# Kernel tuning notes

Measured on AMD Instinct MI355X. Metric: run time of the kernel, lower is better.

## Reference

```python
import jax, jax.numpy as jnp
import numpy as np

EPS = 1e-5

def _layernorm(x, gamma, beta):
    # normalize over last (channel) axis, per point
    mu = jnp.mean(x, axis=-1, keepdims=True)
    var = jnp.mean(jnp.square(x - mu), axis=-1, keepdims=True)
    return (x - mu) * jax.lax.rsqrt(var + EPS) * gamma + beta

def setup_inputs() -> dict:
    key = jax.random.key(0)
    ks = jax.random.split(key, 12)
    B, N, C, F = 32, 4096, 3, 1024
    points = jax.random.normal(ks[0], (B, N, C), dtype=jnp.float32)
    mask = jax.random.randint(ks[1], (B, 1, N), 0, 2, dtype=jnp.int32)
    s = 0.05
    return {
        "points": points,
        "mask": mask,
        "w1": jax.random.normal(ks[2], (128, C), dtype=jnp.float32) * s,      # conv1 (no bias)
        "g1": jnp.ones((128,), jnp.float32),                                   # norm1 gamma
        "be1": jnp.zeros((128,), jnp.float32),                                 # norm1 beta
        "w2": jax.random.normal(ks[3], (256, 128), dtype=jnp.float32) * s,     # conv2
        "b2": jax.random.normal(ks[4], (256,), dtype=jnp.float32) * s,
        "w3": jax.random.normal(ks[5], (512, 512), dtype=jnp.float32) * s,     # conv3 (no bias)
        "g2": jnp.ones((512,), jnp.float32),                                   # norm2 gamma
        "be2": jnp.zeros((512,), jnp.float32),                                 # norm2 beta
        "w4": jax.random.normal(ks[6], (F, 512), dtype=jnp.float32) * s,       # conv4
        "b4": jax.random.normal(ks[7], (F,), dtype=jnp.float32) * s,
    }

def reference(points, mask, w1, g1, be1, w2, b2, w3, g2, be2, w4, b4):
    # points: [B, N, C]; mask: [B, 1, N]
    vis = (mask[:, 0, :] != 0).astype(points.dtype)[..., None]  # [B, N, 1]
    # conv1 (1x1, no bias) as point-wise matmul
    h0 = jnp.einsum('bnc,kc->bnk', points, w1)                  # [B, N, 128]
    # masked LayerNorm: LN is per-point over channels, so compute densely and zero invisible points
    h1 = _layernorm(h0, g1, be1) * vis
    h2 = jax.nn.relu(h1)
    h3 = jnp.einsum('bnk,ok->bno', h2, w2) + b2                 # [B, N, 256]
    gmax = jnp.max(h3, axis=1, keepdims=True)                   # [B, 1, 256]
    dist = jnp.concatenate([jnp.broadcast_to(gmax, h3.shape), h3], axis=-1)  # [B, N, 512]
    h4 = jnp.einsum('bno,po->bnp', dist, w3)                    # [B, N, 512]
    h5 = _layernorm(h4, g2, be2) * vis
    h6 = jax.nn.relu(h5)
    h7 = jnp.einsum('bnp,fp->bnf', h6, w4) + b4                 # [B, N, F]
    return jnp.max(h7, axis=1)                                  # [B, F]
```

## Files before the change

kernel.cpp:

```cpp
#include <hip/hip_runtime.h>
#include <stdint.h>

#define LN_EPS 1e-5f

static __device__ __forceinline__ unsigned short f2bf_bits(float f) {
  union { float f; unsigned u; } v; v.f = f;
  unsigned r = v.u + 0x7FFFu + ((v.u >> 16) & 1u);
  return (unsigned short)(r >> 16);
}
static __device__ __forceinline__ float bf2f(unsigned short h) {
  union { unsigned u; float f; } v; v.u = ((unsigned)h) << 16;
  return v.f;
}

typedef __bf16 bf16x8 __attribute__((ext_vector_type(8)));
typedef float floatx4 __attribute__((ext_vector_type(4)));

typedef __attribute__((address_space(1))) unsigned int* gas_ptr;
typedef __attribute__((address_space(3))) unsigned int* las_ptr;
static __device__ __forceinline__ void async_cp16(const void* g, void* l) {
  __builtin_amdgcn_global_load_lds((gas_ptr)g, (las_ptr)l, 16, 0, 0);
}

__global__ __launch_bounds__(256) void perm_kernel(
    const int* __restrict__ mask, int* __restrict__ newrow, int* __restrict__ cnt) {
  const int b = blockIdx.x, t = threadIdx.x;
  const int base = b * 4096 + t * 16;
  int v[16]; int s = 0;
#pragma unroll
  for (int i = 0; i < 16; ++i) { v[i] = (mask[base + i] != 0); s += v[i]; }
  const int lane = t & 63, wv = t >> 6;
  int scan = s;
  for (int o = 1; o < 64; o <<= 1) { int x = __shfl_up(scan, o); if (lane >= o) scan += x; }
  __shared__ int wsum[4], woff[4], stotal;
  if (lane == 63) wsum[wv] = scan;
  __syncthreads();
  if (t == 0) { int a = 0; for (int k = 0; k < 4; ++k) { woff[k] = a; a += wsum[k]; } stotal = a; cnt[b] = a; }
  __syncthreads();
  const int excl = scan - s + woff[wv];
  const int total = stotal;
  int run = 0;
#pragma unroll
  for (int i = 0; i < 16; ++i) {
    const int pos = t * 16 + i;
    const int visBefore = excl + run;
    newrow[b * 4096 + pos] = v[i] ? visBefore : total + (pos - visBefore);
    run += v[i];
  }
}

__global__ __launch_bounds__(256) void conv1_ln_kernel(
    const float* __restrict__ points,
    const float* __restrict__ w1, const float* __restrict__ g1,
    const float* __restrict__ be1, unsigned short* __restrict__ h2,
    const int* __restrict__ newrow, const int* __restrict__ cnt,
    const float* __restrict__ w2, const float* __restrict__ b2,
    const float* __restrict__ w3, const float* __restrict__ w4,
    unsigned short* __restrict__ w2b, unsigned short* __restrict__ w4b,
    unsigned short* __restrict__ w23b, float* __restrict__ vecb,
    int* __restrict__ hdr, unsigned short* __restrict__ tl128,
    unsigned short* __restrict__ tl256) {
  if (blockIdx.x >= 32768) {
    const int bb = blockIdx.x - 32768;
    if (bb < 2176) {
      int idx = bb * 256 + threadIdx.x;
      if (idx < 32768) w2b[idx] = f2bf_bits(w2[idx]);
      else w4b[idx - 32768] = f2bf_bits(w4[idx - 32768]);
    } else if (bb < 2176 + 256) {
      const int tid = threadIdx.x;
      const int p = (bb - 2176) * 2 + (tid >> 7);
      const int c = tid & 127;
      const float* w3r = w3 + (size_t)p * 512 + 256;
      float s = 0.f;
      for (int k = 0; k < 256; ++k) s += w3r[k] * w2[k * 128 + c];
      w23b[p * 128 + c] = f2bf_bits(s);
      if (c == 0) {
        float vb = 0.f;
        for (int k = 0; k < 256; ++k) vb += w3r[k] * b2[k];
        vecb[p] = vb;
      }
    } else {
      const int lane = threadIdx.x;
      if (lane < 64) {
        const int c = (lane < 32) ? cnt[lane] : 0;
        const int n128 = (c + 127) >> 7;
        const int n256 = (c + 255) >> 8;
        int s128 = n128, s256 = n256;
        for (int o = 1; o < 64; o <<= 1) {
          int x = __shfl_up(s128, o); if (lane >= o) s128 += x;
          int y = __shfl_up(s256, o); if (lane >= o) s256 += y;
        }
        if (lane == 31) { hdr[0] = s128; hdr[1] = s256; }
        if (lane < 32) {
          const int e128 = s128 - n128, e256 = s256 - n256;
          for (int j = 0; j < n128; ++j) tl128[e128 + j] = (unsigned short)(lane * 32 + j);
          for (int j = 0; j < n256; ++j) tl256[e256 + j] = (unsigned short)(lane * 16 + j);
        }
      }
    }
    return;
  }
  const int lane = threadIdx.x & 63;
  const int wv = threadIdx.x >> 6;
  const size_t p = (size_t)blockIdx.x * 4 + wv;
  const int dest = newrow[p];
  const int cntb = cnt[p >> 12];
  const int ceilv = (cntb + 127) & ~127;
  if (dest >= ceilv) return;
  const bool vis = (dest < cntb);
  const float x0 = points[p * 3 + 0];
  const float x1 = points[p * 3 + 1];
  const float x2 = points[p * 3 + 2];
  const int c0 = lane * 2, c1 = c0 + 1;
  float h00 = w1[c0 * 3] * x0 + w1[c0 * 3 + 1] * x1 + w1[c0 * 3 + 2] * x2;
  float h01 = w1[c1 * 3] * x0 + w1[c1 * 3 + 1] * x1 + w1[c1 * 3 + 2] * x2;
  float s = h00 + h01;
  for (int o = 32; o; o >>= 1) s += __shfl_xor(s, o);
  const float mu = s * (1.f / 128.f);
  const float d0 = h00 - mu, d1 = h01 - mu;
  float q = d0 * d0 + d1 * d1;
  for (int o = 32; o; o >>= 1) q += __shfl_xor(q, o);
  const float rs = rsqrtf(q * (1.f / 128.f) + LN_EPS);
  const float y0 = vis ? fmaxf(d0 * rs * g1[c0] + be1[c0], 0.f) : 0.f;
  const float y1 = vis ? fmaxf(d1 * rs * g1[c1] + be1[c1], 0.f) : 0.f;
  union { unsigned u; unsigned short s2[2]; } pk;
  pk.s2[0] = f2bf_bits(y0);
  pk.s2[1] = f2bf_bits(y1);
  const size_t prow = (p & ~(size_t)4095) + (size_t)dest;
  ((unsigned*)h2)[prow * 64 + lane] = pk.u;
}

__global__ __launch_bounds__(256) void gemm23_fused(
    const unsigned short* __restrict__ A,
    const unsigned short* __restrict__ w2b, const unsigned short* __restrict__ w23b,
    unsigned short* __restrict__ h46, float* __restrict__ pg,
    const float* __restrict__ b2, const float* __restrict__ vecb,
    const int* __restrict__ hdr, const unsigned short* __restrict__ tl128) {
  __shared__ __align__(16) char smA[2][128 * 64];
  __shared__ __align__(16) char smB[2][128 * 64];
  __shared__ float lmax[2][128];

  const int nW = hdr[0] * 6;
  const int cw = (nW + 7) >> 3;
  const int slot = blockIdx.x >> 3;
  const int wI = (blockIdx.x & 7) * cw + slot;
  if (slot >= cw || wI >= nW) return;
  const int t6 = wI / 6;
  const int colTile = wI - t6 * 6;
  const int rowTile = tl128[t6];

  const int tid = threadIdx.x;
  const int lane = tid & 63;
  const int w = tid >> 6;
  const int wm = w >> 1, wn = w & 1;

  const bool isPG = (colTile < 2);
  const int colBase = isPG ? colTile * 128 : (colTile - 2) * 128;
  const size_t rowBase = (size_t)rowTile * 128;
  const unsigned short* Bw = isPG ? w2b : w23b;

  floatx4 acc[4][4];
  const floatx4 zero = {0.f, 0.f, 0.f, 0.f};
#pragma unroll
  for (int i = 0; i < 4; ++i)
#pragma unroll
    for (int j = 0; j < 4; ++j) acc[i][j] = zero;

  const int rSub = lane >> 2;
  const int cb16 = (lane & 3) * 16;
  const size_t Kb = 256;
  const char* gA = (const char*)A + (rowBase + (size_t)(w * 32 + rSub)) * Kb + cb16;
  const char* gB = (const char*)Bw + ((size_t)colBase + (size_t)(w * 32 + rSub)) * Kb + cb16;
  char* lA0 = smA[0] + w * 2048;
  char* lA1 = smA[1] + w * 2048;
  char* lB0 = smB[0] + w * 2048;
  char* lB1 = smB[1] + w * 2048;
  const size_t skip16 = 16 * Kb;

  const int fm = lane & 15, fq = lane >> 4;
  const int fOff = fm * 64 + fq * 16;
  const char* pa0 = smA[0] + wm * 64 * 64 + fOff;
  const char* pa1 = smA[1] + wm * 64 * 64 + fOff;
  const char* pb0 = smB[0] + wn * 64 * 64 + fOff;
  const char* pb1 = smB[1] + wn * 64 * 64 + fOff;

  for (int k0 = 0; k0 < 128; k0 += 64) {
    async_cp16(gA, lA0);
    async_cp16(gA + skip16, lA0 + 1024);
    async_cp16(gA + 64, lA1);
    async_cp16(gA + 64 + skip16, lA1 + 1024);
    async_cp16(gB, lB0);
    async_cp16(gB + skip16, lB0 + 1024);
    async_cp16(gB + 64, lB1);
    async_cp16(gB + 64 + skip16, lB1 + 1024);
    gA += 128; gB += 128;
    __syncthreads();
    bf16x8 af0[4], bg0[4], af1[4], bg1[4];
#pragma unroll
    for (int i = 0; i < 4; ++i) af0[i] = *(const bf16x8*)(pa0 + i * 16 * 64);
#pragma unroll
    for (int j = 0; j < 4; ++j) bg0[j] = *(const bf16x8*)(pb0 + j * 16 * 64);
#pragma unroll
    for (int i = 0; i < 4; ++i)
#pragma unroll
      for (int j = 0; j < 4; ++j)
        acc[i][j] = __builtin_amdgcn_mfma_f32_16x16x32_bf16(af0[i], bg0[j], acc[i][j], 0, 0, 0);
#pragma unroll
    for (int i = 0; i < 4; ++i) af1[i] = *(const bf16x8*)(pa1 + i * 16 * 64);
#pragma unroll
    for (int j = 0; j < 4; ++j) bg1[j] = *(const bf16x8*)(pb1 + j * 16 * 64);
#pragma unroll
    for (int i = 0; i < 4; ++i)
#pragma unroll
      for (int j = 0; j < 4; ++j)
        acc[i][j] = __builtin_amdgcn_mfma_f32_16x16x32_bf16(af1[i], bg1[j], acc[i][j], 0, 0, 0);
    __syncthreads();
  }

  if (isPG) {
    float m4[4] = {-1e30f, -1e30f, -1e30f, -1e30f};
#pragma unroll
    for (int j = 0; j < 4; ++j) {
      const float ex = b2[colBase + wn * 64 + j * 16 + fm];
#pragma unroll
      for (int i = 0; i < 4; ++i)
#pragma unroll
        for (int r = 0; r < 4; ++r) m4[j] = fmaxf(m4[j], acc[i][j][r] + ex);
      m4[j] = fmaxf(m4[j], __shfl_xor(m4[j], 16));
      m4[j] = fmaxf(m4[j], __shfl_xor(m4[j], 32));
    }
    const float sel = (fq == 0) ? m4[0] : (fq == 1) ? m4[1] : (fq == 2) ? m4[2] : m4[3];
    lmax[wm][wn * 64 + fq * 16 + fm] = sel;
    __syncthreads();
    if (tid < 128) {
      const float v = fmaxf(lmax[0][tid], lmax[1][tid]);
      pg[(size_t)rowTile * 256 + colBase + tid] = v;
    }
  } else {
#pragma unroll
    for (int j = 0; j < 4; ++j) {
      const int col = colBase + wn * 64 + j * 16 + fm;
      const float ex = vecb[col];
#pragma unroll
      for (int i = 0; i < 4; ++i) {
        const size_t row0 = rowBase + wm * 64 + i * 16 + fq * 4;
#pragma unroll
        for (int r = 0; r < 4; ++r) {
          h46[(row0 + r) * 512 + col] = f2bf_bits(acc[i][j][r] + ex);
        }
      }
    }
  }
}

#define G4_BAR() __builtin_amdgcn_s_barrier()
#define G4_LGKM0() asm volatile("s_waitcnt lgkmcnt(0)" ::: "memory")
#define G4_LGKM8() asm volatile("s_waitcnt lgkmcnt(8)" ::: "memory")
#define G4_VM2() asm volatile("s_waitcnt vmcnt(2)" ::: "memory")
#define G4_VM0() asm volatile("s_waitcnt vmcnt(0)" ::: "memory")
#define G4_PRIO1() __builtin_amdgcn_s_setprio(1)
#define G4_PRIO0() __builtin_amdgcn_s_setprio(0)

#define G4_STG(bufi, h4, kt) do { \
  const char* _s = (((h4) < 2) ? srcA : srcB) + (size_t)((h4) & 1) * (128 * 1024) + (size_t)(kt) * 128; \
  char* _d = stDst + (bufi) * 65536 + ((h4) >> 1) * 32768 + ((h4) & 1) * 16384; \
  async_cp16(_s, _d); \
  async_cp16(_s + 64 * 1024, _d + 8192); \
} while (0)

#define G4_LDA(bufi, mh) do { \
  const char* _p = rdA + (bufi) * 65536 + (mh) * 8192; \
  af[0][0] = *(const bf16x8*)(_p + c0);        af[0][1] = *(const bf16x8*)(_p + c1); \
  af[1][0] = *(const bf16x8*)(_p + 2048 + c0); af[1][1] = *(const bf16x8*)(_p + 2048 + c1); \
  af[2][0] = *(const bf16x8*)(_p + 4096 + c0); af[2][1] = *(const bf16x8*)(_p + 4096 + c1); \
  af[3][0] = *(const bf16x8*)(_p + 6144 + c0); af[3][1] = *(const bf16x8*)(_p + 6144 + c1); \
} while (0)

#define G4_LDB(bufi, nh, bgx) do { \
  const char* _p = rdB + (bufi) * 65536 + (nh) * 4096; \
  bgx[0][0] = *(const bf16x8*)(_p + c0);        bgx[0][1] = *(const bf16x8*)(_p + c1); \
  bgx[1][0] = *(const bf16x8*)(_p + 2048 + c0); bgx[1][1] = *(const bf16x8*)(_p + 2048 + c1); \
} while (0)

#define G4_QUAD(mh, nh, bgx) do { \
  _Pragma("unroll") \
  for (int _m = 0; _m < 4; ++_m) { \
    _Pragma("unroll") \
    for (int _n = 0; _n < 2; ++_n) { \
      acc[(mh) * 4 + _m][(nh) * 2 + _n] = __builtin_amdgcn_mfma_f32_16x16x32_bf16( \
          af[_m][0], bgx[_n][0], acc[(mh) * 4 + _m][(nh) * 2 + _n], 0, 0, 0); \
      acc[(mh) * 4 + _m][(nh) * 2 + _n] = __builtin_amdgcn_mfma_f32_16x16x32_bf16( \
          af[_m][1], bgx[_n][1], acc[(mh) * 4 + _m][(nh) * 2 + _n], 0, 0, 0); \
    } \
  } \
} while (0)

__global__ __launch_bounds__(512, 2) void gemm4_8ph(
    const unsigned short* __restrict__ A, const unsigned short* __restrict__ Bw,
    float* __restrict__ outp2, const int* __restrict__ hdr,
    const unsigned short* __restrict__ tl256) {
  extern __shared__ char sm[];

  const int nW = hdr[1] * 4;
  const int cw = (nW + 7) >> 3;
  const int slot = blockIdx.x >> 3;
  const int wI = (blockIdx.x & 7) * cw + slot;
  if (slot >= cw || wI >= nW) return;
  const int rowTile = tl256[wI >> 2];
  const int colTile = wI & 3;

  const int tid = threadIdx.x;
  const int lane = tid & 63;
  const int w = tid >> 6;
  const int wm = w >> 2, wn = w & 3;

  const size_t rowBase = (size_t)rowTile * 256;
  const int colBase = colTile * 256;

  const int rr = tid >> 3;
  const int csw = ((tid & 7) ^ (rr & 7)) << 4;
  const char* srcA = (const char*)A + (rowBase + (size_t)rr) * 1024 + csw;
  const char* srcB = (const char*)Bw + ((size_t)colBase + (size_t)rr) * 1024 + csw;
  char* stDst = sm + w * 1024;

  const int fr = lane & 15, fq = lane >> 4;
  const int c0 = (fq * 16) ^ ((lane & 7) << 4);
  const int c1 = ((fq * 16) | 64) ^ ((lane & 7) << 4);
  const char* rdA = sm + (wm * 128 + fr) * 128;
  const char* rdB = sm + 32768 + (wn * 64 + fr) * 128;

  floatx4 acc[8][4];
  const floatx4 zero = {0.f, 0.f, 0.f, 0.f};
#pragma unroll
  for (int i = 0; i < 8; ++i)
#pragma unroll
    for (int j = 0; j < 4; ++j) acc[i][j] = zero;

  bf16x8 af[4][2], bg0[2][2], bg1[2][2];

  G4_STG(0, 0, 0); G4_STG(0, 1, 0); G4_STG(0, 2, 0); G4_STG(0, 3, 0);
  G4_STG(1, 0, 1);
  G4_VM2(); G4_BAR();

  for (int it = 0; it < 3; ++it) {
    const int tO = 2 * it + 1, tE2 = 2 * it + 2, tO2 = 2 * it + 3;
    G4_LDA(0, 0); G4_LDB(0, 0, bg0); G4_STG(1, 1, tO); G4_LGKM8(); G4_BAR(); G4_LGKM0();
    G4_PRIO1(); G4_QUAD(0, 0, bg0); G4_PRIO0(); G4_BAR();
    G4_LDB(0, 1, bg1); G4_STG(1, 2, tO); G4_BAR(); G4_LGKM0();
    G4_PRIO1(); G4_QUAD(0, 1, bg1); G4_PRIO0(); G4_BAR();
    G4_LDA(0, 1); G4_STG(1, 3, tO); G4_BAR(); G4_LGKM0();
    G4_PRIO1(); G4_QUAD(1, 1, bg1); G4_PRIO0(); G4_BAR();
    G4_STG(0, 0, tE2); G4_VM2(); G4_BAR();
    G4_PRIO1(); G4_QUAD(1, 0, bg0); G4_PRIO0(); G4_BAR();
    G4_LDA(1, 0); G4_LDB(1, 0, bg0); G4_STG(0, 1, tE2); G4_LGKM8(); G4_BAR(); G4_LGKM0();
    G4_PRIO1(); G4_QUAD(0, 0, bg0); G4_PRIO0(); G4_BAR();
    G4_LDB(1, 1, bg1); G4_STG(0, 2, tE2); G4_BAR(); G4_LGKM0();
    G4_PRIO1(); G4_QUAD(0, 1, bg1); G4_PRIO0(); G4_BAR();
    G4_LDA(1, 1); G4_STG(0, 3, tE2); G4_BAR(); G4_LGKM0();
    G4_PRIO1(); G4_QUAD(1, 1, bg1); G4_PRIO0(); G4_BAR();
    G4_STG(1, 0, tO2); G4_VM2(); G4_BAR();
    G4_PRIO1(); G4_QUAD(1, 0, bg0); G4_PRIO0(); G4_BAR();
  }

  G4_LDA(0, 0); G4_LDB(0, 0, bg0); G4_STG(1, 1, 7); G4_LGKM8(); G4_BAR(); G4_LGKM0();
  G4_PRIO1(); G4_QUAD(0, 0, bg0); G4_PRIO0(); G4_BAR();
  G4_LDB(0, 1, bg1); G4_STG(1, 2, 7); G4_BAR(); G4_LGKM0();
  G4_PRIO1(); G4_QUAD(0, 1, bg1); G4_PRIO0(); G4_BAR();
  G4_LDA(0, 1); G4_STG(1, 3, 7); G4_BAR(); G4_LGKM0();
  G4_PRIO1(); G4_QUAD(1, 1, bg1); G4_PRIO0(); G4_BAR();
  G4_VM0(); G4_BAR();
  G4_PRIO1(); G4_QUAD(1, 0, bg0); G4_PRIO0(); G4_BAR();
  G4_LDA(1, 0); G4_LDB(1, 0, bg0); G4_BAR(); G4_LGKM0();
  G4_PRIO1(); G4_QUAD(0, 0, bg0); G4_PRIO0(); G4_BAR();
  G4_LDB(1, 1, bg1); G4_BAR(); G4_LGKM0();
  G4_PRIO1(); G4_QUAD(0, 1, bg1); G4_PRIO0(); G4_BAR();
  G4_LDA(1, 1); G4_BAR(); G4_LGKM0();
  G4_PRIO1(); G4_QUAD(1, 1, bg1); G4_PRIO0(); G4_BAR();
  G4_PRIO1(); G4_QUAD(1, 0, bg0); G4_PRIO0(); G4_BAR();

  float* smf = (float*)sm;
  float mv[4];
#pragma unroll
  for (int nj = 0; nj < 4; ++nj) {
    float m = -1e30f;
#pragma unroll
    for (int mi = 0; mi < 8; ++mi)
#pragma unroll
      for (int r = 0; r < 4; ++r) m = fmaxf(m, acc[mi][nj][r]);
    m = fmaxf(m, __shfl_xor(m, 16));
    m = fmaxf(m, __shfl_xor(m, 32));
    mv[nj] = m;
  }
  const float sel = (fq == 0) ? mv[0] : (fq == 1) ? mv[1] : (fq == 2) ? mv[2] : mv[3];
  smf[wm * 256 + wn * 64 + fq * 16 + fr] = sel;
  __syncthreads();
  if (tid < 256) {
    outp2[(size_t)rowTile * 1024 + colBase + tid] = fmaxf(smf[tid], smf[256 + tid]);
  }
}

__global__ __launch_bounds__(256) void gmax_cvec_kernel(
    const float* __restrict__ pg, const float* __restrict__ w3,
    float* __restrict__ cvec, const int* __restrict__ cnt,
    const float* __restrict__ b2) {
  __shared__ float gm[256];
  const int b = blockIdx.x >> 2, quarter = blockIdx.x & 3;
  const int t = threadIdx.x;
  const int c = cnt[b];
  const int nt = (c + 127) >> 7;
  float m = (c < 4096) ? b2[t] : -1e30f;
  for (int s = 0; s < nt; ++s) m = fmaxf(m, pg[((size_t)b * 32 + s) * 256 + t]);
  gm[t] = m;
  __syncthreads();
  const int lane = t & 63, wv = t >> 6;
  const float g0 = gm[lane * 4 + 0];
  const float g1 = gm[lane * 4 + 1];
  const float g2v = gm[lane * 4 + 2];
  const float g3 = gm[lane * 4 + 3];
  for (int pp = 0; pp < 32; ++pp) {
    const int p = quarter * 128 + wv * 32 + pp;
    const float4 wr = *(const float4*)(w3 + (size_t)p * 512 + lane * 4);
    float s = wr.x * g0 + wr.y * g1 + wr.z * g2v + wr.w * g3;
    for (int o = 32; o; o >>= 1) s += __shfl_xor(s, o);
    if (lane == 0) cvec[b * 512 + p] = s;
  }
}

__global__ __launch_bounds__(256) void ln2_kernel(
    unsigned short* __restrict__ h46, const int* __restrict__ cnt,
    const float* __restrict__ cvec,
    const float* __restrict__ g2, const float* __restrict__ be2,
    const int* __restrict__ hdr, const unsigned short* __restrict__ tl256) {
  const int nW = hdr[1] * 64;
  if (blockIdx.x >= nW) return;
  const int rowTile = tl256[blockIdx.x >> 6];
  const int lane = threadIdx.x & 63;
  const int wv = threadIdx.x >> 6;
  const size_t p = (size_t)rowTile * 256 + ((blockIdx.x & 63) * 4 + wv);
  const int b = rowTile >> 4;
  const int cb = cnt[b];
  const int pin = (int)(p & 4095);
  unsigned short* row = h46 + p * 512;
  const int c0 = lane * 8;
  if (pin >= cb) {
    const uint4 z = {0, 0, 0, 0};
    *(uint4*)(row + c0) = z;
    return;
  }
  union { uint4 v; unsigned short s[8]; } in;
  in.v = *(const uint4*)(row + c0);
  float cv[8];
  *(float4*)(cv) = *(const float4*)(cvec + b * 512 + c0);
  *(float4*)(cv + 4) = *(const float4*)(cvec + b * 512 + c0 + 4);
  float f[8];
  float s = 0.f;
#pragma unroll
  for (int k = 0; k < 8; ++k) { f[k] = bf2f(in.s[k]) + cv[k]; s += f[k]; }
  for (int o = 32; o; o >>= 1) s += __shfl_xor(s, o);
  const float mu = s * (1.f / 512.f);
  float q = 0.f;
#pragma unroll
  for (int k = 0; k < 8; ++k) { const float d = f[k] - mu; q += d * d; }
  for (int o = 32; o; o >>= 1) q += __shfl_xor(q, o);
  const float rs = rsqrtf(q * (1.f / 512.f) + LN_EPS);
  union { uint4 v; unsigned short s[8]; } outv;
#pragma unroll
  for (int k = 0; k < 8; ++k) {
    const float y = fmaxf((f[k] - mu) * rs * g2[c0 + k] + be2[c0 + k], 0.f);
    outv.s[k] = f2bf_bits(y);
  }
  *(uint4*)(row + c0) = outv.v;
}

__global__ __launch_bounds__(256) void final_kernel(
    const float* __restrict__ pmax, const float* __restrict__ b4,
    float* __restrict__ out, const int* __restrict__ cnt) {
  const int idx = blockIdx.x * 256 + threadIdx.x;
  const int b = idx >> 10, f = idx & 1023;
  const int c = cnt[b];
  const int nt = (c + 255) >> 8;
  float m = (c < 4096) ? 0.f : -1e30f;
  for (int r = 0; r < nt; ++r) m = fmaxf(m, pmax[((size_t)(b * 16 + r)) * 1024 + f]);
  out[idx] = m + b4[f];
}

extern "C" void kernel_launch(void* const* d_in, const int* in_sizes, int n_in,
                              void* d_out, int out_size, void* d_ws, size_t ws_size,
                              hipStream_t stream) {
  const float* points = (const float*)d_in[0];
  const int* mask = (const int*)d_in[1];
  const float* w1 = (const float*)d_in[2];
  const float* g1 = (const float*)d_in[3];
  const float* be1 = (const float*)d_in[4];
  const float* w2 = (const float*)d_in[5];
  const float* b2 = (const float*)d_in[6];
  const float* w3 = (const float*)d_in[7];
  const float* g2 = (const float*)d_in[8];
  const float* be2 = (const float*)d_in[9];
  const float* w4 = (const float*)d_in[10];
  const float* b4 = (const float*)d_in[11];
  float* out = (float*)d_out;
  char* ws = (char*)d_ws;

  const size_t OFF_H46 = 0;
  const size_t OFF_H2 = 134217728;
  const size_t OFF_W2B = OFF_H2 + 33554432;
  const size_t OFF_W4B = OFF_W2B + 65536;
  const size_t OFF_W23B = OFF_W4B + 1048576;
  const size_t OFF_VECB = OFF_W23B + 131072;
  const size_t OFF_PG = OFF_VECB + 2048;
  const size_t OFF_CVEC = OFF_PG + 1048576;
  const size_t OFF_PMAX = OFF_CVEC + 65536;
  const size_t OFF_CNT = OFF_PMAX + 4194304;
  const size_t OFF_NEWROW = OFF_CNT + 4096;
  const size_t OFF_HDR = OFF_NEWROW + 524288;
  const size_t OFF_TL128 = OFF_HDR + 64;
  const size_t OFF_TL256 = OFF_TL128 + 2048;

  unsigned short* h2 = (unsigned short*)(ws + OFF_H2);
  unsigned short* h46 = (unsigned short*)(ws + OFF_H46);
  unsigned short* w2b = (unsigned short*)(ws + OFF_W2B);
  unsigned short* w4b = (unsigned short*)(ws + OFF_W4B);
  unsigned short* w23b = (unsigned short*)(ws + OFF_W23B);
  float* vecb = (float*)(ws + OFF_VECB);
  float* pg = (float*)(ws + OFF_PG);
  float* cvecp = (float*)(ws + OFF_CVEC);
  float* pmaxp = (float*)(ws + OFF_PMAX);
  int* cntp = (int*)(ws + OFF_CNT);
  int* newrow = (int*)(ws + OFF_NEWROW);
  int* hdr = (int*)(ws + OFF_HDR);
  unsigned short* tl128 = (unsigned short*)(ws + OFF_TL128);
  unsigned short* tl256 = (unsigned short*)(ws + OFF_TL256);

  static bool s_attr_done = false;
  if (!s_attr_done) {
    hipFuncSetAttribute((const void*)gemm4_8ph,
                        hipFuncAttributeMaxDynamicSharedMemorySize, 131072);
    s_attr_done = true;
  }

  perm_kernel<<<32, 256, 0, stream>>>(mask, newrow, cntp);
  conv1_ln_kernel<<<32768 + 2176 + 256 + 1, 256, 0, stream>>>(
      points, w1, g1, be1, h2, newrow, cntp, w2, b2, w3, w4, w2b, w4b, w23b, vecb,
      hdr, tl128, tl256);
  gemm23_fused<<<6144, 256, 0, stream>>>(h2, w2b, w23b, h46, pg, b2, vecb, hdr, tl128);
  gmax_cvec_kernel<<<128, 256, 0, stream>>>(pg, w3, cvecp, cntp, b2);
  ln2_kernel<<<32768, 256, 0, stream>>>(h46, cntp, cvecp, g2, be2, hdr, tl256);
  gemm4_8ph<<<2048, 512, 131072, stream>>>(h46, w4b, pmaxp, hdr, tl256);
  final_kernel<<<128, 256, 0, stream>>>(pmaxp, b4, out, cntp);
}
```

Baseline: 275.6 us.

## Fuse gmax/cvec and LN2 into one cooperative kernel; simplify gemm4 tile mapping

Merges the global-max/cvec kernel and the LN2 kernel into a single cooperative launch of 1024 blocks. The first 128 blocks compute cvec, a grid-wide sync follows, and then all blocks run a grid-stride loop over the LN2 rows. This removes one kernel launch and boundary. gemm4 now maps blocks to row tiles directly by XCD, using the per-batch point count to skip empty tiles instead of reading the compacted tile list. The cost is a grid-sync barrier, a lower-occupancy persistent LN2 loop, and a fixed-grid gemm4 that depends on rows being sorted with valid points first.

```diff
diff --git a/kernel.cpp b/kernel.cpp
--- a/kernel.cpp
+++ b/kernel.cpp
@@ -1,5 +1,8 @@
 #include <hip/hip_runtime.h>
+#include <hip/hip_cooperative_groups.h>
 #include <stdint.h>
+
+namespace cg = cooperative_groups;
 
 #define LN_EPS 1e-5f
 
@@ -297,25 +300,25 @@
 
 __global__ __launch_bounds__(512, 2) void gemm4_8ph(
     const unsigned short* __restrict__ A, const unsigned short* __restrict__ Bw,
-    float* __restrict__ outp2, const int* __restrict__ hdr,
-    const unsigned short* __restrict__ tl256) {
+    float* __restrict__ outp2, const int* __restrict__ cnt) {
   extern __shared__ char sm[];
 
-  const int nW = hdr[1] * 4;
-  const int cw = (nW + 7) >> 3;
-  const int slot = blockIdx.x >> 3;
-  const int wI = (blockIdx.x & 7) * cw + slot;
-  if (slot >= cw || wI >= nW) return;
-  const int rowTile = tl256[wI >> 2];
-  const int colTile = wI & 3;
+  const int gid = blockIdx.x;
+  const int xcd = gid & 7;
+  const int slot = gid >> 3;
+  const int rowTile = xcd * 64 + (slot >> 2);
+  const int colTile = slot & 3;
+  const size_t rowBase = (size_t)rowTile * 256;
+  const int colBase = colTile * 256;
+
+  const int cntb = cnt[rowBase >> 12];
+  const int rb = (int)(rowBase & 4095);
+  if (rb >= cntb) return;
 
   const int tid = threadIdx.x;
   const int lane = tid & 63;
   const int w = tid >> 6;
   const int wm = w >> 2, wn = w & 3;
-
-  const size_t rowBase = (size_t)rowTile * 256;
-  const int colBase = colTile * 256;
 
   const int rr = tid >> 3;
   const int csw = ((tid & 7) ^ (rr & 7)) << 4;
@@ -399,77 +402,78 @@
   }
 }
 
-__global__ __launch_bounds__(256) void gmax_cvec_kernel(
+__global__ __launch_bounds__(256, 4) void gmax_ln2_kernel(
     const float* __restrict__ pg, const float* __restrict__ w3,
     float* __restrict__ cvec, const int* __restrict__ cnt,
-    const float* __restrict__ b2) {
-  __shared__ float gm[256];
-  const int b = blockIdx.x >> 2, quarter = blockIdx.x & 3;
-  const int t = threadIdx.x;
-  const int c = cnt[b];
-  const int nt = (c + 127) >> 7;
-  float m = (c < 4096) ? b2[t] : -1e30f;
-  for (int s = 0; s < nt; ++s) m = fmaxf(m, pg[((size_t)b * 32 + s) * 256 + t]);
-  gm[t] = m;
-  __syncthreads();
-  const int lane = t & 63, wv = t >> 6;
-  const float g0 = gm[lane * 4 + 0];
-  const float g1 = gm[lane * 4 + 1];
-  const float g2v = gm[lane * 4 + 2];
-  const float g3 = gm[lane * 4 + 3];
-  for (int pp = 0; pp < 32; ++pp) {
-    const int p = quarter * 128 + wv * 32 + pp;
-    const float4 wr = *(const float4*)(w3 + (size_t)p * 512 + lane * 4);
-    float s = wr.x * g0 + wr.y * g1 + wr.z * g2v + wr.w * g3;
-    for (int o = 32; o; o >>= 1) s += __shfl_xor(s, o);
-    if (lane == 0) cvec[b * 512 + p] = s;
-  }
-}
-
-__global__ __launch_bounds__(256) void ln2_kernel(
-    unsigned short* __restrict__ h46, const int* __restrict__ cnt,
-    const float* __restrict__ cvec,
+    const float* __restrict__ b2,
+    unsigned short* __restrict__ h46,
     const float* __restrict__ g2, const float* __restrict__ be2,
     const int* __restrict__ hdr, const unsigned short* __restrict__ tl256) {
+  __shared__ float gm[256];
+  const int t = threadIdx.x;
+  const int lane = t & 63, wv = t >> 6;
+
+  if (blockIdx.x < 128) {
+    const int b = blockIdx.x >> 2, quarter = blockIdx.x & 3;
+    const int c = cnt[b];
+    const int nt = (c + 127) >> 7;
+    float m = (c < 4096) ? b2[t] : -1e30f;
+    for (int s = 0; s < nt; ++s) m = fmaxf(m, pg[((size_t)b * 32 + s) * 256 + t]);
+    gm[t] = m;
+    __syncthreads();
+    const float g0 = gm[lane * 4 + 0];
+    const float g1 = gm[lane * 4 + 1];
+    const float g2v = gm[lane * 4 + 2];
+    const float g3 = gm[lane * 4 + 3];
+    for (int pp = 0; pp < 32; ++pp) {
+      const int p = quarter * 128 + wv * 32 + pp;
+      const float4 wr = *(const float4*)(w3 + (size_t)p * 512 + lane * 4);
+      float s = wr.x * g0 + wr.y * g1 + wr.z * g2v + wr.w * g3;
+      for (int o = 32; o; o >>= 1) s += __shfl_xor(s, o);
+      if (lane == 0) cvec[b * 512 + p] = s;
+    }
+    __threadfence();
+  }
+  cg::this_grid().sync();
+
   const int nW = hdr[1] * 64;
-  if (blockIdx.x >= nW) return;
-  const int rowTile = tl256[blockIdx.x >> 6];
-  const int lane = threadIdx.x & 63;
-  const int wv = threadIdx.x >> 6;
-  const size_t p = (size_t)rowTile * 256 + ((blockIdx.x & 63) * 4 + wv);
-  const int b = rowTile >> 4;
-  const int cb = cnt[b];
-  const int pin = (int)(p & 4095);
-  unsigned short* row = h46 + p * 512;
-  const int c0 = lane * 8;
-  if (pin >= cb) {
-    const uint4 z = {0, 0, 0, 0};
-    *(uint4*)(row + c0) = z;
-    return;
-  }
-  union { uint4 v; unsigned short s[8]; } in;
-  in.v = *(const uint4*)(row + c0);
-  float cv[8];
-  *(float4*)(cv) = *(const float4*)(cvec + b * 512 + c0);
-  *(float4*)(cv + 4) = *(const float4*)(cvec + b * 512 + c0 + 4);
-  float f[8];
-  float s = 0.f;
-#pragma unroll
-  for (int k = 0; k < 8; ++k) { f[k] = bf2f(in.s[k]) + cv[k]; s += f[k]; }
-  for (int o = 32; o; o >>= 1) s += __shfl_xor(s, o);
-  const float mu = s * (1.f / 512.f);
-  float q = 0.f;
-#pragma unroll
-  for (int k = 0; k < 8; ++k) { const float d = f[k] - mu; q += d * d; }
-  for (int o = 32; o; o >>= 1) q += __shfl_xor(q, o);
-  const float rs = rsqrtf(q * (1.f / 512.f) + LN_EPS);
-  union { uint4 v; unsigned short s[8]; } outv;
-#pragma unroll
-  for (int k = 0; k < 8; ++k) {
-    const float y = fmaxf((f[k] - mu) * rs * g2[c0 + k] + be2[c0 + k], 0.f);
-    outv.s[k] = f2bf_bits(y);
-  }
-  *(uint4*)(row + c0) = outv.v;
+  for (int item = blockIdx.x; item < nW; item += 1024) {
+    const int rowTile = tl256[item >> 6];
+    const size_t p = (size_t)rowTile * 256 + ((item & 63) * 4 + wv);
+    const int b = rowTile >> 4;
+    const int cb = cnt[b];
+    const int pin = (int)(p & 4095);
+    unsigned short* row = h46 + p * 512;
+    const int c0 = lane * 8;
+    if (pin >= cb) {
+      const uint4 z = {0, 0, 0, 0};
+      *(uint4*)(row + c0) = z;
+      continue;
+    }
+    union { uint4 v; unsigned short s[8]; } in;
+    in.v = *(const uint4*)(row + c0);
+    float cv[8];
+    *(float4*)(cv) = *(const float4*)(cvec + b * 512 + c0);
+    *(float4*)(cv + 4) = *(const float4*)(cvec + b * 512 + c0 + 4);
+    float f[8];
+    float s = 0.f;
+#pragma unroll
+    for (int k = 0; k < 8; ++k) { f[k] = bf2f(in.s[k]) + cv[k]; s += f[k]; }
+    for (int o = 32; o; o >>= 1) s += __shfl_xor(s, o);
+    const float mu = s * (1.f / 512.f);
+    float q = 0.f;
+#pragma unroll
+    for (int k = 0; k < 8; ++k) { const float d = f[k] - mu; q += d * d; }
+    for (int o = 32; o; o >>= 1) q += __shfl_xor(q, o);
+    const float rs = rsqrtf(q * (1.f / 512.f) + LN_EPS);
+    union { uint4 v; unsigned short s[8]; } outv;
+#pragma unroll
+    for (int k = 0; k < 8; ++k) {
+      const float y = fmaxf((f[k] - mu) * rs * g2[c0 + k] + be2[c0 + k], 0.f);
+      outv.s[k] = f2bf_bits(y);
+    }
+    *(uint4*)(row + c0) = outv.v;
+  }
 }
 
 __global__ __launch_bounds__(256) void final_kernel(
@@ -544,8 +548,12 @@
       points, w1, g1, be1, h2, newrow, cntp, w2, b2, w3, w4, w2b, w4b, w23b, vecb,
       hdr, tl128, tl256);
   gemm23_fused<<<6144, 256, 0, stream>>>(h2, w2b, w23b, h46, pg, b2, vecb, hdr, tl128);
-  gmax_cvec_kernel<<<128, 256, 0, stream>>>(pg, w3, cvecp, cntp, b2);
-  ln2_kernel<<<32768, 256, 0, stream>>>(h46, cntp, cvecp, g2, be2, hdr, tl256);
-  gemm4_8ph<<<2048, 512, 131072, stream>>>(h46, w4b, pmaxp, hdr, tl256);
+  {
+    void* kargs[] = {(void*)&pg, (void*)&w3, (void*)&cvecp, (void*)&cntp, (void*)&b2,
+                     (void*)&h46, (void*)&g2, (void*)&be2, (void*)&hdr, (void*)&tl256};
+    hipLaunchCooperativeKernel((void*)gmax_ln2_kernel, dim3(1024), dim3(256),
+                               kargs, 0, stream);
+  }
+  gemm4_8ph<<<2048, 512, 131072, stream>>>(h46, w4b, pmaxp, cntp);
   final_kernel<<<128, 256, 0, stream>>>(pmaxp, b4, out, cntp);
 }
```

Result: slower. 367.1 us (+33.2%).

## Fuse final max reduction into gemm4 via last-block atomic counter

Applied to the files above, without the earlier changes.

Removes the separate final_kernel launch. The last gemm4 block to finish for each batch, found through an atomic counter reset in perm_kernel, reduces the partial maxima and writes the output. Row and column tile indices are now derived directly from blockIdx with a per-batch count check, instead of the compacted tile list. This saves a launch and the tile-list indirection, but adds threadfences and an atomic per block. The XCD-major block mapping may also change load balance across XCDs.

```diff
diff --git a/kernel.cpp b/kernel.cpp
--- a/kernel.cpp
+++ b/kernel.cpp
@@ -23,7 +23,8 @@
 }
 
 __global__ __launch_bounds__(256) void perm_kernel(
-    const int* __restrict__ mask, int* __restrict__ newrow, int* __restrict__ cnt) {
+    const int* __restrict__ mask, int* __restrict__ newrow, int* __restrict__ cnt,
+    int* __restrict__ bcnt) {
   const int b = blockIdx.x, t = threadIdx.x;
   const int base = b * 4096 + t * 16;
   int v[16]; int s = 0;
@@ -35,7 +36,10 @@
   __shared__ int wsum[4], woff[4], stotal;
   if (lane == 63) wsum[wv] = scan;
   __syncthreads();
-  if (t == 0) { int a = 0; for (int k = 0; k < 4; ++k) { woff[k] = a; a += wsum[k]; } stotal = a; cnt[b] = a; }
+  if (t == 0) {
+    int a = 0; for (int k = 0; k < 4; ++k) { woff[k] = a; a += wsum[k]; }
+    stotal = a; cnt[b] = a; bcnt[b] = 0;
+  }
   __syncthreads();
   const int excl = scan - s + woff[wv];
   const int total = stotal;
@@ -297,25 +301,27 @@
 
 __global__ __launch_bounds__(512, 2) void gemm4_8ph(
     const unsigned short* __restrict__ A, const unsigned short* __restrict__ Bw,
-    float* __restrict__ outp2, const int* __restrict__ hdr,
-    const unsigned short* __restrict__ tl256) {
+    float* __restrict__ outp2, const int* __restrict__ cnt,
+    int* __restrict__ bcnt, const float* __restrict__ b4,
+    float* __restrict__ out) {
   extern __shared__ char sm[];
 
-  const int nW = hdr[1] * 4;
-  const int cw = (nW + 7) >> 3;
-  const int slot = blockIdx.x >> 3;
-  const int wI = (blockIdx.x & 7) * cw + slot;
-  if (slot >= cw || wI >= nW) return;
-  const int rowTile = tl256[wI >> 2];
-  const int colTile = wI & 3;
+  const int gid = blockIdx.x;
+  const int xcd = gid & 7;
+  const int slot = gid >> 3;
+  const int rowTile = xcd * 64 + (slot >> 2);
+  const int colTile = slot & 3;
+  const size_t rowBase = (size_t)rowTile * 256;
+  const int colBase = colTile * 256;
+
+  const int cntb = cnt[rowBase >> 12];
+  const int rb = (int)(rowBase & 4095);
+  if (rb >= cntb) return;
 
   const int tid = threadIdx.x;
   const int lane = tid & 63;
   const int w = tid >> 6;
   const int wm = w >> 2, wn = w & 3;
-
-  const size_t rowBase = (size_t)rowTile * 256;
-  const int colBase = colTile * 256;
 
   const int rr = tid >> 3;
   const int csw = ((tid & 7) ^ (rr & 7)) << 4;
@@ -396,6 +402,27 @@
   __syncthreads();
   if (tid < 256) {
     outp2[(size_t)rowTile * 1024 + colBase + tid] = fmaxf(smf[tid], smf[256 + tid]);
+  }
+
+  __threadfence();
+  __syncthreads();
+  int* flagp = (int*)(sm + 8192);
+  const int b = (int)(rowBase >> 12);
+  const int ntb = (cntb + 255) >> 8;
+  if (tid == 0) {
+    const int prev = atomicAdd(&bcnt[b], 1);
+    *flagp = (prev == ntb * 4 - 1) ? 1 : 0;
+  }
+  __syncthreads();
+  if (*flagp) {
+    __threadfence();
+    const float basev = (cntb < 4096) ? 0.f : -1e30f;
+    for (int f0 = tid; f0 < 1024; f0 += 512) {
+      float m = basev;
+      for (int r = 0; r < ntb; ++r)
+        m = fmaxf(m, outp2[((size_t)(b * 16 + r)) * 1024 + f0]);
+      out[b * 1024 + f0] = m + b4[f0];
+    }
   }
 }
 
@@ -472,18 +499,6 @@
   *(uint4*)(row + c0) = outv.v;
 }
 
-__global__ __launch_bounds__(256) void final_kernel(
-    const float* __restrict__ pmax, const float* __restrict__ b4,
-    float* __restrict__ out, const int* __restrict__ cnt) {
-  const int idx = blockIdx.x * 256 + threadIdx.x;
-  const int b = idx >> 10, f = idx & 1023;
-  const int c = cnt[b];
-  const int nt = (c + 255) >> 8;
-  float m = (c < 4096) ? 0.f : -1e30f;
-  for (int r = 0; r < nt; ++r) m = fmaxf(m, pmax[((size_t)(b * 16 + r)) * 1024 + f]);
-  out[idx] = m + b4[f];
-}
-
 extern "C" void kernel_launch(void* const* d_in, const int* in_sizes, int n_in,
                               void* d_out, int out_size, void* d_ws, size_t ws_size,
                               hipStream_t stream) {
@@ -516,6 +531,7 @@
   const size_t OFF_HDR = OFF_NEWROW + 524288;
   const size_t OFF_TL128 = OFF_HDR + 64;
   const size_t OFF_TL256 = OFF_TL128 + 2048;
+  const size_t OFF_BCNT = OFF_TL256 + 1024;
 
   unsigned short* h2 = (unsigned short*)(ws + OFF_H2);
   unsigned short* h46 = (unsigned short*)(ws + OFF_H46);
@@ -531,6 +547,7 @@
   int* hdr = (int*)(ws + OFF_HDR);
   unsigned short* tl128 = (unsigned short*)(ws + OFF_TL128);
   unsigned short* tl256 = (unsigned short*)(ws + OFF_TL256);
+  int* bcntp = (int*)(ws + OFF_BCNT);
 
   static bool s_attr_done = false;
   if (!s_attr_done) {
@@ -539,13 +556,12 @@
     s_attr_done = true;
   }
 
-  perm_kernel<<<32, 256, 0, stream>>>(mask, newrow, cntp);
+  perm_kernel<<<32, 256, 0, stream>>>(mask, newrow, cntp, bcntp);
   conv1_ln_kernel<<<32768 + 2176 + 256 + 1, 256, 0, stream>>>(
       points, w1, g1, be1, h2, newrow, cntp, w2, b2, w3, w4, w2b, w4b, w23b, vecb,
       hdr, tl128, tl256);
   gemm23_fused<<<6144, 256, 0, stream>>>(h2, w2b, w23b, h46, pg, b2, vecb, hdr, tl128);
   gmax_cvec_kernel<<<128, 256, 0, stream>>>(pg, w3, cvecp, cntp, b2);
   ln2_kernel<<<32768, 256, 0, stream>>>(h46, cntp, cvecp, g2, be2, hdr, tl256);
-  gemm4_8ph<<<2048, 512, 131072, stream>>>(h46, w4b, pmaxp, hdr, tl256);
-  final_kernel<<<128, 256, 0, stream>>>(pmaxp, b4, out, cntp);
-}
+  gemm4_8ph<<<2048, 512, 131072, stream>>>(h46, w4b, pmaxp, cntp, bcntp, b4, out);
+}
```

Result: slower. 411.6 us (+49.4%).
